# Performance work log

Hardware: AMD Instinct MI355X
Metric: run time of the kernel (lower is better)

Reference implementation:

```python
import jax, jax.numpy as jnp
import numpy as np

B, SRC, PRED, D = 256, 512, 128, 512  # D = hidden_size * 2


def setup_inputs() -> dict:
    key = jax.random.key(0)
    k1, k2, k3, k4 = jax.random.split(key, 4)
    enc_out = jax.random.normal(k1, (B, SRC, D), dtype=jnp.float32)
    dec_out = jax.random.normal(k2, (B, PRED, D), dtype=jnp.float32)
    attn_mask = jax.random.randint(k3, (B, SRC), 0, 2).astype(jnp.bool_)
    # nn.Linear(D, D, bias=False) weight, torch layout (out, in)
    W = jax.random.normal(k4, (D, D), dtype=jnp.float32) * (1.0 / np.sqrt(D))
    return {"enc_out": enc_out, "dec_out": dec_out, "attn_mask": attn_mask, "W": W}


def reference(enc_out, dec_out, attn_mask, W):
    # query = dec_out @ W.T  (torch Linear)
    query = jnp.einsum('bpd,ed->bpe', dec_out, W)           # (B, PRED, D)
    # unscaled Luong scores
    scores = jnp.einsum('bpd,bsd->bps', query, enc_out)     # (B, PRED, SRC)
    scores = jnp.where(attn_mask[:, None, :], -jnp.inf, scores)
    weight = jax.nn.softmax(scores, axis=-1)
    context = jnp.einsum('bps,bsd->bpd', weight, enc_out)   # (B, PRED, D)
    return context
```

## Files before the change

kernel.cpp:

```cpp
#include <hip/hip_runtime.h>
#include <hip/hip_bf16.h>
#include <stdint.h>

#define NB    256
#define NSRC  512
#define NPRED 128
#define ND    512

typedef float  f32x4  __attribute__((ext_vector_type(4)));
typedef short  bf16x8 __attribute__((ext_vector_type(8)));
typedef unsigned short u16;
typedef unsigned int   u32;

__device__ __forceinline__ u16 bf16_rne(float x) {
    u32 u = __float_as_uint(x);
    u32 r = (u + 0x7FFFu + ((u >> 16) & 1u)) >> 16;
    return (u16)r;
}
__device__ __forceinline__ float bf2f(u16 h) {
    return __uint_as_float(((u32)h) << 16);
}

#define K1ROW 72

__global__ __launch_bounds__(256, 2)
void k_query(const float* __restrict__ dec, const float* __restrict__ W,
             u32* __restrict__ qout)
{
    extern __shared__ u16 lds1[];
    u16* Ah = lds1;
    u16* Al = Ah + 128 * K1ROW;
    u16* Bh = Al + 128 * K1ROW;
    u16* Bl = Bh + 128 * K1ROW;

    int bid = blockIdx.x;
    int wg  = (bid & 7) * 128 + (bid >> 3);
    int tm  = wg >> 2;
    int tn  = wg & 3;
    int tid  = threadIdx.x;
    int lane = tid & 63;
    int wid  = tid >> 6;
    int wr = wid >> 1, wc = wid & 1;
    int ln = lane & 15, lg = lane >> 4;

    f32x4 acc[4][4];
#pragma unroll
    for (int i = 0; i < 4; ++i)
#pragma unroll
        for (int j = 0; j < 4; ++j) { acc[i][j][0]=0.f; acc[i][j][1]=0.f; acc[i][j][2]=0.f; acc[i][j][3]=0.f; }

    float4 pva[8], pvb[8];
#pragma unroll
    for (int i = 0; i < 8; ++i) {
        int flat = (i * 256 + tid) * 4;
        int r = flat >> 6, c = flat & 63;
        pva[i] = *(const float4*)(dec + (size_t)(tm * 128 + r) * 512 + 0 * 64 + c);
        pvb[i] = *(const float4*)(W   + (size_t)(tn * 128 + r) * 512 + 0 * 64 + c);
    }

    for (int kt = 0; kt < 8; ++kt) {
        if (kt) __syncthreads();
#pragma unroll
        for (int i = 0; i < 8; ++i) {
            int flat = (i * 256 + tid) * 4;
            int r = flat >> 6, c = flat & 63;
            float4 va = pva[i];
            ushort4 h, l;
            h.x = bf16_rne(va.x); l.x = bf16_rne(va.x - bf2f(h.x));
            h.y = bf16_rne(va.y); l.y = bf16_rne(va.y - bf2f(h.y));
            h.z = bf16_rne(va.z); l.z = bf16_rne(va.z - bf2f(h.z));
            h.w = bf16_rne(va.w); l.w = bf16_rne(va.w - bf2f(h.w));
            *(ushort4*)(Ah + r * K1ROW + c) = h;
            *(ushort4*)(Al + r * K1ROW + c) = l;
            float4 vb = pvb[i];
            ushort4 hb, lb;
            hb.x = bf16_rne(vb.x); lb.x = bf16_rne(vb.x - bf2f(hb.x));
            hb.y = bf16_rne(vb.y); lb.y = bf16_rne(vb.y - bf2f(hb.y));
            hb.z = bf16_rne(vb.z); lb.z = bf16_rne(vb.z - bf2f(hb.z));
            hb.w = bf16_rne(vb.w); lb.w = bf16_rne(vb.w - bf2f(hb.w));
            *(ushort4*)(Bh + r * K1ROW + c) = hb;
            *(ushort4*)(Bl + r * K1ROW + c) = lb;
        }
        __syncthreads();
        if (kt < 7) {
#pragma unroll
            for (int i = 0; i < 8; ++i) {
                int flat = (i * 256 + tid) * 4;
                int r = flat >> 6, c = flat & 63;
                pva[i] = *(const float4*)(dec + (size_t)(tm * 128 + r) * 512 + (kt + 1) * 64 + c);
                pvb[i] = *(const float4*)(W   + (size_t)(tn * 128 + r) * 512 + (kt + 1) * 64 + c);
            }
        }
#pragma unroll
        for (int ks = 0; ks < 2; ++ks) {
            int ko = ks * 32 + lg * 8;
            bf16x8 ah[4], al[4], bh[4], bl[4];
#pragma unroll
            for (int ms = 0; ms < 4; ++ms) {
                int m = wr * 64 + ms * 16 + ln;
                ah[ms] = *(const bf16x8*)(Ah + m * K1ROW + ko);
                al[ms] = *(const bf16x8*)(Al + m * K1ROW + ko);
            }
#pragma unroll
            for (int ns = 0; ns < 4; ++ns) {
                int n = wc * 64 + ns * 16 + ln;
                bh[ns] = *(const bf16x8*)(Bh + n * K1ROW + ko);
                bl[ns] = *(const bf16x8*)(Bl + n * K1ROW + ko);
            }
#pragma unroll
            for (int ms = 0; ms < 4; ++ms)
#pragma unroll
                for (int ns = 0; ns < 4; ++ns) {
                    acc[ms][ns] = __builtin_amdgcn_mfma_f32_16x16x32_bf16(ah[ms], bh[ns], acc[ms][ns], 0, 0, 0);
                    acc[ms][ns] = __builtin_amdgcn_mfma_f32_16x16x32_bf16(ah[ms], bl[ns], acc[ms][ns], 0, 0, 0);
                    acc[ms][ns] = __builtin_amdgcn_mfma_f32_16x16x32_bf16(al[ms], bh[ns], acc[ms][ns], 0, 0, 0);
                }
        }
    }
#pragma unroll
    for (int ms = 0; ms < 4; ++ms)
#pragma unroll
        for (int ns = 0; ns < 4; ++ns)
#pragma unroll
            for (int j = 0; j < 4; ++j) {
                int r = tm * 128 + wr * 64 + ms * 16 + lg * 4 + j;
                int c = tn * 128 + wc * 64 + ns * 16 + ln;
                float v = acc[ms][ns][j];
                u16 hi = bf16_rne(v);
                u16 lo = bf16_rne(v - bf2f(hi));
                qout[(size_t)r * 512 + c] = ((u32)hi << 16) | (u32)lo;
            }
}

#define QROW 72
#define EROW 72
#define WROW 528
#define TROW 40

__global__ __launch_bounds__(512, 2)
void k_attn(const float* __restrict__ enc, const u32* qpk,
            const void* __restrict__ maskraw, float* out)
{
    extern __shared__ char smem[];
    u16* Qh = (u16*)smem;
    u16* Ql = Qh + 64 * QROW;
    u16* Eh = Ql + 64 * QROW;
    u16* El = Eh + 128 * EROW;
    u16* wlds  = (u16*)smem;
    u16* eldsT = (u16*)(smem + 64 * WROW * 2);
    float* scrM = (float*)(smem + 64 * WROW * 2 + 512 * TROW * 2);
    float* scrS = scrM + 128;
    int* flagsh = (int*)(scrS + 128);

    int tid  = threadIdx.x;
    int lane = tid & 63, wid = tid >> 6;
    int wm = wid >> 1, wn = wid & 1;
    int ln = lane & 15, lg = lane >> 4;

    int bid = blockIdx.x;
    int wg  = (bid & 7) * 64 + (bid >> 3);
    int b   = wg >> 1;
    int ph  = wg & 1;
    int brow0 = b * 128 + ph * 64;

    const int* mi = (const int*)maskraw;
    int bad = 0;
    for (int i = tid; i < 1024; i += 512) {
        int v = mi[i];
        if (!(v == 0 || v == 1 || v == 0x3F800000)) bad = 1;
    }
    if (tid == 0) *flagsh = 0;
    __syncthreads();
    if (bad) atomicOr(flagsh, 1);
    __syncthreads();
    const int mbyte = *flagsh;

    f32x4 acc[16];
#pragma unroll
    for (int t = 0; t < 16; ++t) { acc[t][0]=0.f; acc[t][1]=0.f; acc[t][2]=0.f; acc[t][3]=0.f; }

    for (int dc = 0; dc < 8; ++dc) {
#pragma unroll
        for (int i = 0; i < 2; ++i) {
            int flat = (i * 512 + tid) * 4;
            int r = flat >> 6, c = flat & 63;
            uint4 v = *(const uint4*)(qpk + (size_t)(brow0 + r) * 512 + dc * 64 + c);
            ushort4 h, l;
            h.x = (u16)(v.x >> 16); l.x = (u16)(v.x & 0xFFFF);
            h.y = (u16)(v.y >> 16); l.y = (u16)(v.y & 0xFFFF);
            h.z = (u16)(v.z >> 16); l.z = (u16)(v.z & 0xFFFF);
            h.w = (u16)(v.w >> 16); l.w = (u16)(v.w & 0xFFFF);
            *(ushort4*)(Qh + r * QROW + c) = h;
            *(ushort4*)(Ql + r * QROW + c) = l;
        }
#pragma unroll
        for (int ns = 0; ns < 4; ++ns) {
#pragma unroll
            for (int i = 0; i < 4; ++i) {
                int flat = (i * 512 + tid) * 4;
                int r = flat >> 6, c = flat & 63;
                float4 v = *(const float4*)(enc + (size_t)(b * 512 + ns * 128 + r) * 512 + dc * 64 + c);
                ushort4 h, l;
                h.x = bf16_rne(v.x); l.x = bf16_rne(v.x - bf2f(h.x));
                h.y = bf16_rne(v.y); l.y = bf16_rne(v.y - bf2f(h.y));
                h.z = bf16_rne(v.z); l.z = bf16_rne(v.z - bf2f(h.z));
                h.w = bf16_rne(v.w); l.w = bf16_rne(v.w - bf2f(h.w));
                *(ushort4*)(Eh + r * EROW + c) = h;
                *(ushort4*)(El + r * EROW + c) = l;
            }
            __syncthreads();
#pragma unroll
            for (int ks = 0; ks < 2; ++ks) {
                int ko = ks * 32 + lg * 8;
                bf16x8 ah = *(const bf16x8*)(Qh + (wm * 16 + ln) * QROW + ko);
                bf16x8 al = *(const bf16x8*)(Ql + (wm * 16 + ln) * QROW + ko);
#pragma unroll
                for (int nb = 0; nb < 4; ++nb) {
                    int n = wn * 64 + nb * 16 + ln;
                    bf16x8 bh = *(const bf16x8*)(Eh + n * EROW + ko);
                    bf16x8 bl = *(const bf16x8*)(El + n * EROW + ko);
                    acc[ns * 4 + nb] = __builtin_amdgcn_mfma_f32_16x16x32_bf16(ah, bh, acc[ns * 4 + nb], 0, 0, 0);
                    acc[ns * 4 + nb] = __builtin_amdgcn_mfma_f32_16x16x32_bf16(ah, bl, acc[ns * 4 + nb], 0, 0, 0);
                    acc[ns * 4 + nb] = __builtin_amdgcn_mfma_f32_16x16x32_bf16(al, bh, acc[ns * 4 + nb], 0, 0, 0);
                }
            }
            __syncthreads();
        }
    }

#pragma unroll
    for (int t = 0; t < 16; ++t) {
        int s = (t >> 2) * 128 + wn * 64 + (t & 3) * 16 + ln;
        bool msk = mbyte ? (((const unsigned char*)maskraw)[b * 512 + s] != 0)
                         : (mi[b * 512 + s] != 0);
        if (msk) { acc[t][0] = -1e30f; acc[t][1] = -1e30f; acc[t][2] = -1e30f; acc[t][3] = -1e30f; }
    }
    int rbase = wm * 16 + lg * 4;
    float mx[4] = { -1e30f, -1e30f, -1e30f, -1e30f };
#pragma unroll
    for (int t = 0; t < 16; ++t)
#pragma unroll
        for (int j = 0; j < 4; ++j) mx[j] = fmaxf(mx[j], acc[t][j]);
#pragma unroll
    for (int d = 1; d < 16; d <<= 1)
#pragma unroll
        for (int j = 0; j < 4; ++j) mx[j] = fmaxf(mx[j], __shfl_xor(mx[j], d, 64));
    if (ln == 0)
#pragma unroll
        for (int j = 0; j < 4; ++j) scrM[wn * 64 + rbase + j] = mx[j];
    __syncthreads();
    float m4[4];
#pragma unroll
    for (int j = 0; j < 4; ++j) m4[j] = fmaxf(scrM[rbase + j], scrM[64 + rbase + j]);
    float sm[4] = { 0.f, 0.f, 0.f, 0.f };
#pragma unroll
    for (int t = 0; t < 16; ++t)
#pragma unroll
        for (int j = 0; j < 4; ++j) {
            float e = __expf(acc[t][j] - m4[j]);
            acc[t][j] = e;
            sm[j] += e;
        }
#pragma unroll
    for (int d = 1; d < 16; d <<= 1)
#pragma unroll
        for (int j = 0; j < 4; ++j) sm[j] += __shfl_xor(sm[j], d, 64);
    if (ln == 0)
#pragma unroll
        for (int j = 0; j < 4; ++j) scrS[wn * 64 + rbase + j] = sm[j];
    __syncthreads();
    float rinv[4];
#pragma unroll
    for (int j = 0; j < 4; ++j) rinv[j] = 1.0f / (scrS[rbase + j] + scrS[64 + rbase + j]);

#pragma unroll
    for (int t = 0; t < 16; ++t) {
        int s = (t >> 2) * 128 + wn * 64 + (t & 3) * 16 + ln;
#pragma unroll
        for (int j = 0; j < 4; ++j)
            wlds[(rbase + j) * WROW + s] = bf16_rne(acc[t][j]);
    }
    __syncthreads();

#pragma unroll
    for (int t = 0; t < 16; ++t) { acc[t][0]=0.f; acc[t][1]=0.f; acc[t][2]=0.f; acc[t][3]=0.f; }

    for (int sc = 0; sc < 16; ++sc) {
        if (sc) __syncthreads();
        {
            int d = tid;
#pragma unroll
            for (int i = 0; i < 8; ++i) {
                size_t base = (size_t)(b * 512 + sc * 32 + i * 4) * 512 + d;
                float v0 = enc[base];
                float v1 = enc[base + 512];
                float v2 = enc[base + 1024];
                float v3 = enc[base + 1536];
                ushort4 h;
                h.x = bf16_rne(v0); h.y = bf16_rne(v1); h.z = bf16_rne(v2); h.w = bf16_rne(v3);
                *(ushort4*)(eldsT + d * TROW + i * 4) = h;
            }
        }
        __syncthreads();
        bf16x8 aw = *(const bf16x8*)(wlds + (wm * 16 + ln) * WROW + sc * 32 + lg * 8);
#pragma unroll
        for (int nb = 0; nb < 16; ++nb) {
            int d = wn * 256 + nb * 16 + ln;
            bf16x8 bv = *(const bf16x8*)(eldsT + d * TROW + lg * 8);
            acc[nb] = __builtin_amdgcn_mfma_f32_16x16x32_bf16(aw, bv, acc[nb], 0, 0, 0);
        }
    }

#pragma unroll
    for (int t = 0; t < 16; ++t) {
        int d = wn * 256 + t * 16 + ln;
#pragma unroll
        for (int j = 0; j < 4; ++j) {
            int p = rbase + j;
            out[(size_t)(brow0 + p) * 512 + d] = acc[t][j] * rinv[j];
        }
    }
}

extern "C" void kernel_launch(void* const* d_in, const int* in_sizes, int n_in,
                              void* d_out, int out_size, void* d_ws, size_t ws_size,
                              hipStream_t stream) {
    const float* enc  = (const float*)d_in[0];
    const float* dec  = (const float*)d_in[1];
    const void*  mask = d_in[2];
    const float* W    = (const float*)d_in[3];
    u32* qpk = (u32*)d_out;

    k_query<<<dim3(1024), dim3(256), 4 * 128 * K1ROW * 2, stream>>>(dec, W, qpk);
    size_t lds2 = (size_t)64 * WROW * 2 + (size_t)512 * TROW * 2 + 2 * 128 * 4 + 16;
    k_attn<<<dim3(512), dim3(512), lds2, stream>>>(enc, qpk, mask, (float*)d_out);
}
```

Before: 703.1 us.

## Prefetch encoder tiles, truncate bf16 splits, shrink query K-tile and LDS padding

Several changes at once. The attention kernel now prefetches the next encoder and query tiles into registers while the current tile is multiplied, and drops one barrier per step. The hi/lo bf16 split switches from round-to-nearest to cheap truncation with packed 32-bit stores. The query GEMM moves to a 32-wide K tile with higher occupancy (launch bounds 3). LDS row pitches for the weight and transpose buffers are retuned, and the latter is read with 64-bit loads. These cut conversion ALU work and global-load stalls, at the cost of more registers and slightly different split precision.

```diff
diff --git a/kernel.cpp b/kernel.cpp
--- a/kernel.cpp
+++ b/kernel.cpp
@@ -17,13 +17,23 @@
     u32 r = (u + 0x7FFFu + ((u >> 16) & 1u)) >> 16;
     return (u16)r;
 }
-__device__ __forceinline__ float bf2f(u16 h) {
-    return __uint_as_float(((u32)h) << 16);
-}
-
-#define K1ROW 72
-
-__global__ __launch_bounds__(256, 2)
+
+__device__ __forceinline__ void split4(float4 v, uint2& hi, uint2& lo) {
+    u32 u0 = __float_as_uint(v.x), u1 = __float_as_uint(v.y);
+    u32 u2 = __float_as_uint(v.z), u3 = __float_as_uint(v.w);
+    hi.x = (u0 >> 16) | (u1 & 0xFFFF0000u);
+    hi.y = (u2 >> 16) | (u3 & 0xFFFF0000u);
+    float r0 = v.x - __uint_as_float(u0 & 0xFFFF0000u);
+    float r1 = v.y - __uint_as_float(u1 & 0xFFFF0000u);
+    float r2 = v.z - __uint_as_float(u2 & 0xFFFF0000u);
+    float r3 = v.w - __uint_as_float(u3 & 0xFFFF0000u);
+    lo.x = (__float_as_uint(r0) >> 16) | (__float_as_uint(r1) & 0xFFFF0000u);
+    lo.y = (__float_as_uint(r2) >> 16) | (__float_as_uint(r3) & 0xFFFF0000u);
+}
+
+#define K1ROW 40
+
+__global__ __launch_bounds__(256, 3)
 void k_query(const float* __restrict__ dec, const float* __restrict__ W,
              u32* __restrict__ qout)
 {
@@ -43,78 +53,67 @@
     int wr = wid >> 1, wc = wid & 1;
     int ln = lane & 15, lg = lane >> 4;
 
+    const float* decb = dec + (size_t)tm * 128 * 512;
+    const float* Wb   = W   + (size_t)tn * 128 * 512;
+
     f32x4 acc[4][4];
 #pragma unroll
     for (int i = 0; i < 4; ++i)
 #pragma unroll
         for (int j = 0; j < 4; ++j) { acc[i][j][0]=0.f; acc[i][j][1]=0.f; acc[i][j][2]=0.f; acc[i][j][3]=0.f; }
 
-    float4 pva[8], pvb[8];
-#pragma unroll
-    for (int i = 0; i < 8; ++i) {
+    float4 pa[4], pb[4];
+#pragma unroll
+    for (int i = 0; i < 4; ++i) {
         int flat = (i * 256 + tid) * 4;
-        int r = flat >> 6, c = flat & 63;
-        pva[i] = *(const float4*)(dec + (size_t)(tm * 128 + r) * 512 + 0 * 64 + c);
-        pvb[i] = *(const float4*)(W   + (size_t)(tn * 128 + r) * 512 + 0 * 64 + c);
-    }
-
-    for (int kt = 0; kt < 8; ++kt) {
+        int r = flat >> 5, c = flat & 31;
+        pa[i] = *(const float4*)(decb + (size_t)r * 512 + c);
+        pb[i] = *(const float4*)(Wb   + (size_t)r * 512 + c);
+    }
+
+    for (int kt = 0; kt < 16; ++kt) {
         if (kt) __syncthreads();
 #pragma unroll
-        for (int i = 0; i < 8; ++i) {
+        for (int i = 0; i < 4; ++i) {
             int flat = (i * 256 + tid) * 4;
-            int r = flat >> 6, c = flat & 63;
-            float4 va = pva[i];
-            ushort4 h, l;
-            h.x = bf16_rne(va.x); l.x = bf16_rne(va.x - bf2f(h.x));
-            h.y = bf16_rne(va.y); l.y = bf16_rne(va.y - bf2f(h.y));
-            h.z = bf16_rne(va.z); l.z = bf16_rne(va.z - bf2f(h.z));
-            h.w = bf16_rne(va.w); l.w = bf16_rne(va.w - bf2f(h.w));
-            *(ushort4*)(Ah + r * K1ROW + c) = h;
-            *(ushort4*)(Al + r * K1ROW + c) = l;
-            float4 vb = pvb[i];
-            ushort4 hb, lb;
-            hb.x = bf16_rne(vb.x); lb.x = bf16_rne(vb.x - bf2f(hb.x));
-            hb.y = bf16_rne(vb.y); lb.y = bf16_rne(vb.y - bf2f(hb.y));
-            hb.z = bf16_rne(vb.z); lb.z = bf16_rne(vb.z - bf2f(hb.z));
-            hb.w = bf16_rne(vb.w); lb.w = bf16_rne(vb.w - bf2f(hb.w));
-            *(ushort4*)(Bh + r * K1ROW + c) = hb;
-            *(ushort4*)(Bl + r * K1ROW + c) = lb;
+            int r = flat >> 5, c = flat & 31;
+            uint2 h, l;
+            split4(pa[i], h, l);
+            *(uint2*)(Ah + r * K1ROW + c) = h;
+            *(uint2*)(Al + r * K1ROW + c) = l;
+            split4(pb[i], h, l);
+            *(uint2*)(Bh + r * K1ROW + c) = h;
+            *(uint2*)(Bl + r * K1ROW + c) = l;
         }
         __syncthreads();
-        if (kt < 7) {
-#pragma unroll
-            for (int i = 0; i < 8; ++i) {
+        if (kt < 15) {
+#pragma unroll
+            for (int i = 0; i < 4; ++i) {
                 int flat = (i * 256 + tid) * 4;
-                int r = flat >> 6, c = flat & 63;
-                pva[i] = *(const float4*)(dec + (size_t)(tm * 128 + r) * 512 + (kt + 1) * 64 + c);
-                pvb[i] = *(const float4*)(W   + (size_t)(tn * 128 + r) * 512 + (kt + 1) * 64 + c);
-            }
-        }
-#pragma unroll
-        for (int ks = 0; ks < 2; ++ks) {
-            int ko = ks * 32 + lg * 8;
-            bf16x8 ah[4], al[4], bh[4], bl[4];
+                int r = flat >> 5, c = flat & 31;
+                pa[i] = *(const float4*)(decb + (size_t)r * 512 + (kt + 1) * 32 + c);
+                pb[i] = *(const float4*)(Wb   + (size_t)r * 512 + (kt + 1) * 32 + c);
+            }
+        }
+        int ko = lg * 8;
+        bf16x8 ah[4], al[4];
+#pragma unroll
+        for (int ms = 0; ms < 4; ++ms) {
+            int m = wr * 64 + ms * 16 + ln;
+            ah[ms] = *(const bf16x8*)(Ah + m * K1ROW + ko);
+            al[ms] = *(const bf16x8*)(Al + m * K1ROW + ko);
+        }
+#pragma unroll
+        for (int ns = 0; ns < 4; ++ns) {
+            int n = wc * 64 + ns * 16 + ln;
+            bf16x8 bh = *(const bf16x8*)(Bh + n * K1ROW + ko);
+            bf16x8 bl = *(const bf16x8*)(Bl + n * K1ROW + ko);
 #pragma unroll
             for (int ms = 0; ms < 4; ++ms) {
-                int m = wr * 64 + ms * 16 + ln;
-                ah[ms] = *(const bf16x8*)(Ah + m * K1ROW + ko);
-                al[ms] = *(const bf16x8*)(Al + m * K1ROW + ko);
-            }
-#pragma unroll
-            for (int ns = 0; ns < 4; ++ns) {
-                int n = wc * 64 + ns * 16 + ln;
-                bh[ns] = *(const bf16x8*)(Bh + n * K1ROW + ko);
-                bl[ns] = *(const bf16x8*)(Bl + n * K1ROW + ko);
-            }
-#pragma unroll
-            for (int ms = 0; ms < 4; ++ms)
-#pragma unroll
-                for (int ns = 0; ns < 4; ++ns) {
-                    acc[ms][ns] = __builtin_amdgcn_mfma_f32_16x16x32_bf16(ah[ms], bh[ns], acc[ms][ns], 0, 0, 0);
-                    acc[ms][ns] = __builtin_amdgcn_mfma_f32_16x16x32_bf16(ah[ms], bl[ns], acc[ms][ns], 0, 0, 0);
-                    acc[ms][ns] = __builtin_amdgcn_mfma_f32_16x16x32_bf16(al[ms], bh[ns], acc[ms][ns], 0, 0, 0);
-                }
+                acc[ms][ns] = __builtin_amdgcn_mfma_f32_16x16x32_bf16(ah[ms], bh, acc[ms][ns], 0, 0, 0);
+                acc[ms][ns] = __builtin_amdgcn_mfma_f32_16x16x32_bf16(ah[ms], bl, acc[ms][ns], 0, 0, 0);
+                acc[ms][ns] = __builtin_amdgcn_mfma_f32_16x16x32_bf16(al[ms], bh, acc[ms][ns], 0, 0, 0);
+            }
         }
     }
 #pragma unroll
@@ -126,16 +125,18 @@
                 int r = tm * 128 + wr * 64 + ms * 16 + lg * 4 + j;
                 int c = tn * 128 + wc * 64 + ns * 16 + ln;
                 float v = acc[ms][ns][j];
-                u16 hi = bf16_rne(v);
-                u16 lo = bf16_rne(v - bf2f(hi));
-                qout[(size_t)r * 512 + c] = ((u32)hi << 16) | (u32)lo;
+                u32 u  = __float_as_uint(v);
+                u32 hi = u >> 16;
+                float rres = v - __uint_as_float(u & 0xFFFF0000u);
+                u32 lo = __float_as_uint(rres) >> 16;
+                qout[(size_t)r * 512 + c] = (hi << 16) | lo;
             }
 }
 
 #define QROW 72
 #define EROW 72
-#define WROW 528
-#define TROW 40
+#define WROW 520
+#define TROW 36
 
 __global__ __launch_bounds__(512, 2)
 void k_attn(const float* __restrict__ enc, const u32* qpk,
@@ -179,36 +180,71 @@
 #pragma unroll
     for (int t = 0; t < 16; ++t) { acc[t][0]=0.f; acc[t][1]=0.f; acc[t][2]=0.f; acc[t][3]=0.f; }
 
+    int eflat = tid * 4;
+    int qr0 = (0 * 512 + tid) * 4 >> 6;
+    float4 pe[4];
+    uint4  pq[2];
+#pragma unroll
+    for (int i = 0; i < 4; ++i) {
+        int flat = (i * 512 + tid) * 4;
+        int r = flat >> 6, c = flat & 63;
+        pe[i] = *(const float4*)(enc + (size_t)(b * 512 + 0 * 128 + r) * 512 + 0 * 64 + c);
+    }
+#pragma unroll
+    for (int i = 0; i < 2; ++i) {
+        int flat = (i * 512 + tid) * 4;
+        int r = flat >> 6, c = flat & 63;
+        pq[i] = *(const uint4*)(qpk + (size_t)(brow0 + r) * 512 + 0 * 64 + c);
+    }
+    (void)eflat; (void)qr0;
+
     for (int dc = 0; dc < 8; ++dc) {
 #pragma unroll
-        for (int i = 0; i < 2; ++i) {
-            int flat = (i * 512 + tid) * 4;
-            int r = flat >> 6, c = flat & 63;
-            uint4 v = *(const uint4*)(qpk + (size_t)(brow0 + r) * 512 + dc * 64 + c);
-            ushort4 h, l;
-            h.x = (u16)(v.x >> 16); l.x = (u16)(v.x & 0xFFFF);
-            h.y = (u16)(v.y >> 16); l.y = (u16)(v.y & 0xFFFF);
-            h.z = (u16)(v.z >> 16); l.z = (u16)(v.z & 0xFFFF);
-            h.w = (u16)(v.w >> 16); l.w = (u16)(v.w & 0xFFFF);
-            *(ushort4*)(Qh + r * QROW + c) = h;
-            *(ushort4*)(Ql + r * QROW + c) = l;
-        }
-#pragma unroll
         for (int ns = 0; ns < 4; ++ns) {
+            if (dc || ns) __syncthreads();
+            if (ns == 0) {
+#pragma unroll
+                for (int i = 0; i < 2; ++i) {
+                    int flat = (i * 512 + tid) * 4;
+                    int r = flat >> 6, c = flat & 63;
+                    uint4 v = pq[i];
+                    uint2 h, l;
+                    h.x = (v.x >> 16) | (v.y & 0xFFFF0000u);
+                    h.y = (v.z >> 16) | (v.w & 0xFFFF0000u);
+                    l.x = (v.x & 0xFFFFu) | (v.y << 16);
+                    l.y = (v.z & 0xFFFFu) | (v.w << 16);
+                    *(uint2*)(Qh + r * QROW + c) = h;
+                    *(uint2*)(Ql + r * QROW + c) = l;
+                }
+            }
 #pragma unroll
             for (int i = 0; i < 4; ++i) {
                 int flat = (i * 512 + tid) * 4;
                 int r = flat >> 6, c = flat & 63;
-                float4 v = *(const float4*)(enc + (size_t)(b * 512 + ns * 128 + r) * 512 + dc * 64 + c);
-                ushort4 h, l;
-                h.x = bf16_rne(v.x); l.x = bf16_rne(v.x - bf2f(h.x));
-                h.y = bf16_rne(v.y); l.y = bf16_rne(v.y - bf2f(h.y));
-                h.z = bf16_rne(v.z); l.z = bf16_rne(v.z - bf2f(h.z));
-                h.w = bf16_rne(v.w); l.w = bf16_rne(v.w - bf2f(h.w));
-                *(ushort4*)(Eh + r * EROW + c) = h;
-                *(ushort4*)(El + r * EROW + c) = l;
+                uint2 h, l;
+                split4(pe[i], h, l);
+                *(uint2*)(Eh + r * EROW + c) = h;
+                *(uint2*)(El + r * EROW + c) = l;
             }
             __syncthreads();
+            if (!(dc == 7 && ns == 3)) {
+                int ndc = (ns == 3) ? dc + 1 : dc;
+                int nns = (ns == 3) ? 0 : ns + 1;
+#pragma unroll
+                for (int i = 0; i < 4; ++i) {
+                    int flat = (i * 512 + tid) * 4;
+                    int r = flat >> 6, c = flat & 63;
+                    pe[i] = *(const float4*)(enc + (size_t)(b * 512 + nns * 128 + r) * 512 + ndc * 64 + c);
+                }
+                if (ns == 3) {
+#pragma unroll
+                    for (int i = 0; i < 2; ++i) {
+                        int flat = (i * 512 + tid) * 4;
+                        int r = flat >> 6, c = flat & 63;
+                        pq[i] = *(const uint4*)(qpk + (size_t)(brow0 + r) * 512 + (dc + 1) * 64 + c);
+                    }
+                }
+            }
 #pragma unroll
             for (int ks = 0; ks < 2; ++ks) {
                 int ko = ks * 32 + lg * 8;
@@ -224,7 +260,6 @@
                     acc[ns * 4 + nb] = __builtin_amdgcn_mfma_f32_16x16x32_bf16(al, bh, acc[ns * 4 + nb], 0, 0, 0);
                 }
             }
-            __syncthreads();
         }
     }
 
@@ -306,8 +341,12 @@
 #pragma unroll
         for (int nb = 0; nb < 16; ++nb) {
             int d = wn * 256 + nb * 16 + ln;
-            bf16x8 bv = *(const bf16x8*)(eldsT + d * TROW + lg * 8);
-            acc[nb] = __builtin_amdgcn_mfma_f32_16x16x32_bf16(aw, bv, acc[nb], 0, 0, 0);
+            const u16* bp = eldsT + d * TROW + lg * 8;
+            uint2 b0 = *(const uint2*)(bp);
+            uint2 b1 = *(const uint2*)(bp + 4);
+            union { uint4 u; bf16x8 v; } cv;
+            cv.u.x = b0.x; cv.u.y = b0.y; cv.u.z = b1.x; cv.u.w = b1.y;
+            acc[nb] = __builtin_amdgcn_mfma_f32_16x16x32_bf16(aw, cv.v, acc[nb], 0, 0, 0);
         }
     }
 
```

Result: faster. 573.0 us (-18.5%).
